# Optimization experiments

Hardware: AMD Instinct MI355X
Metric: run time of the kernel (lower is better)

Reference implementation:

```python
import jax, jax.numpy as jnp
import numpy as np

HIDDEN = 1024
NUM_HEADS = 16
HEAD_DIM = HIDDEN // NUM_HEADS
ROPE_BASE = 10000.0
LN_EPS = 1e-8


def _rope_cos_sin(seq_len, dim, dtype=jnp.float32):
    inv_freq = 1.0 / (ROPE_BASE ** (jnp.arange(0, dim, 2, dtype=jnp.float32) / dim))
    t = jnp.arange(seq_len, dtype=jnp.float32)
    freqs = jnp.einsum('i,j->ij', t, inv_freq)          # [S, dim/2]
    emb = jnp.concatenate([freqs, freqs], axis=-1)       # [S, dim]
    return jnp.cos(emb).astype(dtype), jnp.sin(emb).astype(dtype)


def _rotate_half(x):
    x1, x2 = jnp.split(x, 2, axis=-1)
    return jnp.concatenate([-x2, x1], axis=-1)


def setup_inputs() -> dict:
    key = jax.random.key(0)
    ks = jax.random.split(key, 8)
    B, S, H = 4, 2048, HIDDEN
    x = jax.random.normal(ks[0], (B, S, H), dtype=jnp.float32)
    # causal mask, True = attend
    attn_mask = jnp.tril(jnp.ones((S, S), dtype=bool))[None].repeat(B, axis=0)
    lim_p = 1.0 / np.sqrt(H)
    Wp = jax.random.uniform(ks[1], (H, 4 * H), minval=-lim_p, maxval=lim_p, dtype=jnp.float32)
    bp = jax.random.uniform(ks[2], (4 * H,), minval=-lim_p, maxval=lim_p, dtype=jnp.float32)
    ln_g = jnp.ones((H,), dtype=jnp.float32)
    ln_b = jnp.zeros((H,), dtype=jnp.float32)
    Wt = jax.random.uniform(ks[3], (H, H), minval=-lim_p, maxval=lim_p, dtype=jnp.float32)
    bt = jax.random.uniform(ks[4], (H,), minval=-lim_p, maxval=lim_p, dtype=jnp.float32)
    return {"x": x, "attn_mask": attn_mask, "Wp": Wp, "bp": bp,
            "ln_g": ln_g, "ln_b": ln_b, "Wt": Wt, "bt": bt}


def reference(x, attn_mask, Wp, bp, ln_g, ln_b, Wt, bt):
    B, S, H = x.shape
    nh, hd = NUM_HEADS, HEAD_DIM
    proj = x @ Wp + bp                                   # [B,S,4H]
    U, V, Q, K = jnp.split(proj, 4, axis=-1)
    # [B, nh, S, hd]
    Q = Q.reshape(B, S, nh, hd).transpose(0, 2, 1, 3)
    K = K.reshape(B, S, nh, hd).transpose(0, 2, 1, 3)
    V = V.reshape(B, S, nh, hd).transpose(0, 2, 1, 3)
    cos, sin = _rope_cos_sin(S, hd, x.dtype)             # [S, hd]
    Qr = Q * cos + _rotate_half(Q) * sin
    Kr = K * cos + _rotate_half(K) * sin
    scale = hd ** -0.5
    scores = jnp.einsum('bhqd,bhkd->bhqk', Qr, Kr) * scale
    # masked positions -> sigmoid(-inf) == 0; use where for grad safety
    attn = jnp.where(attn_mask[:, None, :, :], jax.nn.sigmoid(scores), 0.0)
    attn_out = jnp.einsum('bhqk,bhkd->bhqd', attn, V)
    attn_out = attn_out.transpose(0, 2, 1, 3).reshape(B, S, H)
    mu = jnp.mean(attn_out, axis=-1, keepdims=True)
    var = jnp.var(attn_out, axis=-1, keepdims=True)
    attn_out = (attn_out - mu) / jnp.sqrt(var + LN_EPS) * ln_g + ln_b
    gated = jax.nn.silu(U) * attn_out
    out = gated @ Wt + bt
    return x + out
```

## Files before the change

### kernel.cpp

```cpp
#include <hip/hip_runtime.h>
#include <math.h>

#define H 1024
#define NH 16
#define HD 64
#define B_ 4
#define S_ 2048
#define ROWS (B_*S_)

#define QSCALE (-0.1803368801111664f)
#define ROPE_C (9.210340371976184f / 32.0f)

typedef __bf16 bf16x2_t __attribute__((ext_vector_type(2)));
typedef __bf16 bf16x4_t __attribute__((ext_vector_type(4)));
typedef __bf16 bf16x8_t __attribute__((ext_vector_type(8)));
typedef float floatx4_t __attribute__((ext_vector_type(4)));

#define GLOAD_LDS16(gp, lp)                                                        \
    __builtin_amdgcn_global_load_lds(                                              \
        (const __attribute__((address_space(1))) unsigned int*)(gp),               \
        (__attribute__((address_space(3))) unsigned int*)(lp), 16, 0, 0)

__global__ __launch_bounds__(256)
void prep_kernel(const float* __restrict__ x, const float* __restrict__ Wp,
                 const float* __restrict__ Wt,
                 __bf16* __restrict__ Ax, __bf16* __restrict__ Wp_t,
                 __bf16* __restrict__ Wt_t)
{
    __shared__ __bf16 t[32][33];
    const int flat = blockIdx.x;
    const int tid = threadIdx.x;

    if (flat < 8192) {
        size_t i = (size_t)flat * 256 + tid;
        float4 v = *reinterpret_cast<const float4*>(&x[i * 4]);
        bf16x4_t w = { (__bf16)v.x, (__bf16)v.y, (__bf16)v.z, (__bf16)v.w };
        *reinterpret_cast<bf16x4_t*>(&Ax[i * 4]) = w;
        return;
    }
    const float* W; __bf16* Wo; int K, N, bn, bk;
    if (flat < 12288) {
        int id = flat - 8192;  W = Wp; Wo = Wp_t; K = 1024; N = 4096;
        bn = (id & 127) * 32;  bk = (id >> 7) * 32;
    } else {
        int id = flat - 12288; W = Wt; Wo = Wt_t; K = 1024; N = 1024;
        bn = (id & 31) * 32;   bk = (id >> 5) * 32;
    }
    const int tx = tid & 31, ty = tid >> 5;
#pragma unroll
    for (int i = 0; i < 4; i++) {
        int r = ty + i * 8;
        t[tx][r] = (__bf16)W[(size_t)(bk + r) * N + bn + tx];
    }
    __syncthreads();
#pragma unroll
    for (int i = 0; i < 4; i++) {
        int r = ty + i * 8;
        Wo[(size_t)(bn + r) * K + bk + tx] = t[r][tx];
    }
}


__global__ __launch_bounds__(256)
void gemm_out(const __bf16* __restrict__ A, const __bf16* __restrict__ Bt,
              const float* __restrict__ bias, const float* __restrict__ resid,
              float* __restrict__ C, int M, int N, int K)
{
    __shared__ __bf16 As[2][4096];
    __shared__ __bf16 Bs[2][4096];

    const int tid  = threadIdx.x;
    const int wave = tid >> 6, lane = tid & 63;
    const int quad = lane >> 4, ln = lane & 15;
    const int wm = wave & 1, wn = wave >> 1;
    const int m0 = blockIdx.y * 128, n0 = blockIdx.x * 128;

    const int srow = lane >> 2;
    const int skc  = (((lane & 3) ^ ((srow >> 1) & 3)) * 8);
    const int qsw  = (quad ^ ((ln >> 1) & 3)) * 8;

    const int i0 = wave * 2, i1 = i0 + 1;
    const size_t ga0 = (size_t)(m0 + i0 * 16 + srow) * K + skc;
    const size_t ga1 = (size_t)(m0 + i1 * 16 + srow) * K + skc;
    const size_t gb0 = (size_t)(n0 + i0 * 16 + srow) * K + skc;
    const size_t gb1 = (size_t)(n0 + i1 * 16 + srow) * K + skc;

    floatx4_t acc[4][4];
#pragma unroll
    for (int i = 0; i < 4; i++)
#pragma unroll
        for (int j = 0; j < 4; j++) acc[i][j] = (floatx4_t){0.f, 0.f, 0.f, 0.f};

    GLOAD_LDS16(A  + ga0, &As[0][i0 * 512]);
    GLOAD_LDS16(A  + ga1, &As[0][i1 * 512]);
    GLOAD_LDS16(Bt + gb0, &Bs[0][i0 * 512]);
    GLOAD_LDS16(Bt + gb1, &Bs[0][i1 * 512]);

    int buf = 0;
    for (int k0 = 0; k0 < K; k0 += 32, buf ^= 1) {
        __syncthreads();
        if (k0 + 32 < K) {
            int nb = buf ^ 1, kn = k0 + 32;
            GLOAD_LDS16(A  + ga0 + kn, &As[nb][i0 * 512]);
            GLOAD_LDS16(A  + ga1 + kn, &As[nb][i1 * 512]);
            GLOAD_LDS16(Bt + gb0 + kn, &Bs[nb][i0 * 512]);
            GLOAD_LDS16(Bt + gb1 + kn, &Bs[nb][i1 * 512]);
        }
        bf16x8_t af[4], bf[4];
#pragma unroll
        for (int mt = 0; mt < 4; mt++)
            af[mt] = *reinterpret_cast<const bf16x8_t*>(&As[buf][(wm * 64 + mt * 16 + ln) * 32 + qsw]);
#pragma unroll
        for (int nt = 0; nt < 4; nt++)
            bf[nt] = *reinterpret_cast<const bf16x8_t*>(&Bs[buf][(wn * 64 + nt * 16 + ln) * 32 + qsw]);
#pragma unroll
        for (int mt = 0; mt < 4; mt++)
#pragma unroll
            for (int nt = 0; nt < 4; nt++)
                acc[mt][nt] = __builtin_amdgcn_mfma_f32_16x16x32_bf16(af[mt], bf[nt], acc[mt][nt], 0, 0, 0);
    }

#pragma unroll
    for (int mt = 0; mt < 4; mt++) {
#pragma unroll
        for (int nt = 0; nt < 4; nt++) {
            int col = n0 + wn * 64 + nt * 16 + ln;
            float bv = bias[col];
#pragma unroll
            for (int reg = 0; reg < 4; reg++) {
                int row = m0 + wm * 64 + mt * 16 + quad * 4 + reg;
                C[(size_t)row * N + col] = acc[mt][nt][reg] + bv + resid[(size_t)row * N + col];
            }
        }
    }
}

__global__ __launch_bounds__(256)
void gemm_proj(const __bf16* __restrict__ A, const __bf16* __restrict__ Bt,
               const float* __restrict__ bias,
               __bf16* __restrict__ Ug, __bf16* __restrict__ Vh,
               __bf16* __restrict__ Qh, __bf16* __restrict__ Kh)
{
    const int K = 1024;
    __shared__ __bf16 As[2][4096];
    __shared__ __bf16 Bs[2][4096];

    const int tid  = threadIdx.x;
    const int wave = tid >> 6, lane = tid & 63;
    const int quad = lane >> 4, ln = lane & 15;
    const int wm = wave & 1, wn = wave >> 1;
    const int m0 = blockIdx.y * 128, n0 = blockIdx.x * 128;

    const int srow = lane >> 2;
    const int skc  = (((lane & 3) ^ ((srow >> 1) & 3)) * 8);
    const int qsw  = (quad ^ ((ln >> 1) & 3)) * 8;

    const int i0 = wave * 2, i1 = i0 + 1;
    const size_t ga0 = (size_t)(m0 + i0 * 16 + srow) * K + skc;
    const size_t ga1 = (size_t)(m0 + i1 * 16 + srow) * K + skc;
    const size_t gb0 = (size_t)(n0 + i0 * 16 + srow) * K + skc;
    const size_t gb1 = (size_t)(n0 + i1 * 16 + srow) * K + skc;

    floatx4_t acc[4][4];
#pragma unroll
    for (int i = 0; i < 4; i++)
#pragma unroll
        for (int j = 0; j < 4; j++) acc[i][j] = (floatx4_t){0.f, 0.f, 0.f, 0.f};

    GLOAD_LDS16(A  + ga0, &As[0][i0 * 512]);
    GLOAD_LDS16(A  + ga1, &As[0][i1 * 512]);
    GLOAD_LDS16(Bt + gb0, &Bs[0][i0 * 512]);
    GLOAD_LDS16(Bt + gb1, &Bs[0][i1 * 512]);

    int buf = 0;
    for (int k0 = 0; k0 < K; k0 += 32, buf ^= 1) {
        __syncthreads();
        if (k0 + 32 < K) {
            int nb = buf ^ 1, kn = k0 + 32;
            GLOAD_LDS16(A  + ga0 + kn, &As[nb][i0 * 512]);
            GLOAD_LDS16(A  + ga1 + kn, &As[nb][i1 * 512]);
            GLOAD_LDS16(Bt + gb0 + kn, &Bs[nb][i0 * 512]);
            GLOAD_LDS16(Bt + gb1 + kn, &Bs[nb][i1 * 512]);
        }
        bf16x8_t af[4], bf[4];
#pragma unroll
        for (int mt = 0; mt < 4; mt++)
            af[mt] = *reinterpret_cast<const bf16x8_t*>(&As[buf][(wm * 64 + mt * 16 + ln) * 32 + qsw]);
#pragma unroll
        for (int nt = 0; nt < 4; nt++)
            bf[nt] = *reinterpret_cast<const bf16x8_t*>(&Bs[buf][(wn * 64 + nt * 16 + ln) * 32 + qsw]);
#pragma unroll
        for (int mt = 0; mt < 4; mt++)
#pragma unroll
            for (int nt = 0; nt < 4; nt++)
                acc[mt][nt] = __builtin_amdgcn_mfma_f32_16x16x32_bf16(af[mt], bf[nt], acc[mt][nt], 0, 0, 0);
    }

    float bv[4];
#pragma unroll
    for (int nt = 0; nt < 4; nt++) bv[nt] = bias[n0 + wn * 64 + nt * 16 + ln];

    if (n0 < 1024) {
#pragma unroll
        for (int mt = 0; mt < 4; mt++)
#pragma unroll
            for (int nt = 0; nt < 4; nt++) {
                int col = n0 + wn * 64 + nt * 16 + ln;
#pragma unroll
                for (int reg = 0; reg < 4; reg++) {
                    int row = m0 + wm * 64 + mt * 16 + quad * 4 + reg;
                    Ug[(size_t)row * 1024 + col] = (__bf16)(acc[mt][nt][reg] + bv[nt]);
                }
            }
    } else if (n0 < 2048) {
        const int h = ((n0 - 1024) >> 6) + wn;
#pragma unroll
        for (int mt = 0; mt < 4; mt++)
#pragma unroll
            for (int reg = 0; reg < 4; reg++) {
                int row = m0 + wm * 64 + mt * 16 + quad * 4 + reg;
                int b = row >> 11, s = row & (S_ - 1);
                size_t orow = ((size_t)(b * NH + h) * S_ + s) * 64;
#pragma unroll
                for (int nt = 0; nt < 4; nt++)
                    Vh[orow + nt * 16 + ln] = (__bf16)(acc[mt][nt][reg] + bv[nt]);
            }
    } else {
        const bool isQ = (n0 < 3072);
        const int h = ((n0 - (isQ ? 2048 : 3072)) >> 6) + wn;
        __bf16* dst = isQ ? Qh : Kh;
        const float sc = isQ ? QSCALE : 1.0f;
        const float inv0 = __expf(-(float)ln * ROPE_C);
        const float inv1 = __expf(-(float)(16 + ln) * ROPE_C);
#pragma unroll
        for (int mt = 0; mt < 4; mt++)
#pragma unroll
            for (int reg = 0; reg < 4; reg++) {
                int row = m0 + wm * 64 + mt * 16 + quad * 4 + reg;
                int b = row >> 11, s = row & (S_ - 1);
                size_t orow = ((size_t)(b * NH + h) * S_ + s) * 64;
                float sn0, cs0, sn1, cs1;
                __sincosf((float)s * inv0, &sn0, &cs0);
                __sincosf((float)s * inv1, &sn1, &cs1);
                float lo0 = acc[mt][0][reg] + bv[0], hi0 = acc[mt][2][reg] + bv[2];
                float lo1 = acc[mt][1][reg] + bv[1], hi1 = acc[mt][3][reg] + bv[3];
                dst[orow + ln]      = (__bf16)((lo0 * cs0 - hi0 * sn0) * sc);
                dst[orow + 32 + ln] = (__bf16)((hi0 * cs0 + lo0 * sn0) * sc);
                dst[orow + 16 + ln] = (__bf16)((lo1 * cs1 - hi1 * sn1) * sc);
                dst[orow + 48 + ln] = (__bf16)((hi1 * cs1 + lo1 * sn1) * sc);
            }
    }
}

__global__ __launch_bounds__(256)
void transpose_v(const __bf16* __restrict__ Vh, __bf16* __restrict__ VtG)
{
    const int tid = threadIdx.x;
    const int st = blockIdx.x, bh = blockIdx.y;
    const int s0 = st * 64;
    const int d = tid & 63, k16 = tid >> 6;
    __bf16 vals[16];
#pragma unroll
    for (int j = 0; j < 16; j++) {
        int k = s0 + k16 * 16 + j;
        vals[j] = Vh[((size_t)bh * S_ + k) * 64 + d];
    }
    size_t orow = ((size_t)(bh * 64 + d)) * S_ + s0 + k16 * 16;
    *reinterpret_cast<bf16x8_t*>(&VtG[orow])     = *reinterpret_cast<bf16x8_t*>(&vals[0]);
    *reinterpret_cast<bf16x8_t*>(&VtG[orow + 8]) = *reinterpret_cast<bf16x8_t*>(&vals[8]);
}

__global__ __launch_bounds__(256)
void attn_mfma(const __bf16* __restrict__ Qh, const __bf16* __restrict__ Kh,
               const __bf16* __restrict__ VtG, __bf16* __restrict__ attn_out)
{
    __shared__ __bf16 Ks[2][4096];
    __shared__ __bf16 Vt[2][4096];
    __shared__ __bf16 Ps[4][16][72];

    const int tid = threadIdx.x, wave = tid >> 6, lane = tid & 63;
    const int quad = lane >> 4, ln = lane & 15;
    const int qt = (S_ / 128 - 1) - (blockIdx.x >> 6);
    const int hb = blockIdx.x & 63, h = hb & 15, b = hb >> 4, bh = b * NH + h;
    const int Q0 = qt * 128, T0 = 2 * qt;
    const int wl = wave * 16 + ln;

    const size_t qr = ((size_t)bh * S_ + Q0 + wl) * 64;
    bf16x8_t qa[2][2];
    qa[0][0] = *reinterpret_cast<const bf16x8_t*>(&Qh[qr + quad * 8]);
    qa[0][1] = *reinterpret_cast<const bf16x8_t*>(&Qh[qr + 32 + quad * 8]);
    qa[1][0] = *reinterpret_cast<const bf16x8_t*>(&Qh[qr + 4096 + quad * 8]);
    qa[1][1] = *reinterpret_cast<const bf16x8_t*>(&Qh[qr + 4096 + 32 + quad * 8]);

    const int sr = lane >> 3, scl = (lane & 7) ^ sr;
    const int c0 = wave * 2, c1 = c0 + 1;
    const size_t khead = (size_t)bh * S_ * 64;
    const int koff0 = (c0 * 8 + sr) * 64 + scl * 8;
    const int koff1 = (c1 * 8 + sr) * 64 + scl * 8;
    const size_t vg0 = ((size_t)bh * 64 + c0 * 8 + sr) * S_ + scl * 8;
    const size_t vg1 = ((size_t)bh * 64 + c1 * 8 + sr) * S_ + scl * 8;

    const int m7 = ln & 7;
    int ka[4][2];
#pragma unroll
    for (int nt = 0; nt < 4; nt++) {
        int row = nt * 16 + ln;
        ka[nt][0] = row * 64 + ((quad ^ m7) << 3);
        ka[nt][1] = row * 64 + (((quad + 4) ^ m7) << 3);
    }

    floatx4_t o[2][4];
#pragma unroll
    for (int s = 0; s < 2; s++)
#pragma unroll
        for (int dt = 0; dt < 4; dt++) o[s][dt] = (floatx4_t){0.f, 0.f, 0.f, 0.f};

    GLOAD_LDS16(Kh  + khead + koff0, &Ks[0][c0 * 512]);
    GLOAD_LDS16(Kh  + khead + koff1, &Ks[0][c1 * 512]);
    GLOAD_LDS16(VtG + vg0,           &Vt[0][c0 * 512]);
    GLOAD_LDS16(VtG + vg1,           &Vt[0][c1 * 512]);

    for (int kt = 0; kt <= T0 + 1; kt++) {
        const int buf = kt & 1;
        __syncthreads();
        if (kt <= T0) {
            const int nb = buf ^ 1;
            const size_t kg = khead + (size_t)(kt + 1) * 4096;
            GLOAD_LDS16(Kh  + kg + koff0,            &Ks[nb][c0 * 512]);
            GLOAD_LDS16(Kh  + kg + koff1,            &Ks[nb][c1 * 512]);
            GLOAD_LDS16(VtG + vg0 + (kt + 1) * 64,   &Vt[nb][c0 * 512]);
            GLOAD_LDS16(VtG + vg1 + (kt + 1) * 64,   &Vt[nb][c1 * 512]);
        }

        bf16x8_t kf[4][2], vf[4][2];
#pragma unroll
        for (int nt = 0; nt < 4; nt++) {
            kf[nt][0] = *reinterpret_cast<const bf16x8_t*>(&Ks[buf][ka[nt][0]]);
            kf[nt][1] = *reinterpret_cast<const bf16x8_t*>(&Ks[buf][ka[nt][1]]);
        }
#pragma unroll
        for (int dt = 0; dt < 4; dt++) {
            vf[dt][0] = *reinterpret_cast<const bf16x8_t*>(&Vt[buf][ka[dt][0]]);
            vf[dt][1] = *reinterpret_cast<const bf16x8_t*>(&Vt[buf][ka[dt][1]]);
        }

        const int mode0 = (kt < T0) ? 0 : ((kt == T0) ? 1 : 2);
        const int mode1 = (kt <= T0) ? 0 : 1;

#pragma unroll
        for (int s = 0; s < 2; s++) {
            const int mode = s ? mode1 : mode0;
            if (mode == 2) continue;

            floatx4_t st[4];
#pragma unroll
            for (int nt = 0; nt < 4; nt++) {
                floatx4_t acc = (floatx4_t){0.f, 0.f, 0.f, 0.f};
                acc = __builtin_amdgcn_mfma_f32_16x16x32_bf16(kf[nt][0], qa[s][0], acc, 0, 0, 0);
                acc = __builtin_amdgcn_mfma_f32_16x16x32_bf16(kf[nt][1], qa[s][1], acc, 0, 0, 0);
                st[nt] = acc;
            }

#pragma unroll
            for (int nt = 0; nt < 4; nt++) {
                bf16x4_t pk;
#pragma unroll
                for (int r = 0; r < 4; r++) {
                    float a = st[nt][r];
                    if (mode == 1) {
                        int kl = nt * 16 + quad * 4 + r;
                        a = (kl <= wl) ? a : __builtin_inff();
                    }
                    float p = __builtin_amdgcn_rcpf(1.f + __builtin_amdgcn_exp2f(a));
                    pk[r] = (__bf16)p;
                }
                *reinterpret_cast<bf16x4_t*>(&Ps[wave][ln][nt * 16 + quad * 4]) = pk;
            }

            const __bf16* prow = &Ps[wave][ln][quad * 8];
            bf16x8_t p0 = *reinterpret_cast<const bf16x8_t*>(prow);
            bf16x8_t p1 = *reinterpret_cast<const bf16x8_t*>(prow + 32);
#pragma unroll
            for (int dt = 0; dt < 4; dt++) {
                o[s][dt] = __builtin_amdgcn_mfma_f32_16x16x32_bf16(p0, vf[dt][0], o[s][dt], 0, 0, 0);
                o[s][dt] = __builtin_amdgcn_mfma_f32_16x16x32_bf16(p1, vf[dt][1], o[s][dt], 0, 0, 0);
            }
        }
    }

#pragma unroll
    for (int s = 0; s < 2; s++) {
        const int qrow_g = b * S_ + Q0 + s * 64 + wave * 16 + quad * 4;
#pragma unroll
        for (int dt = 0; dt < 4; dt++) {
#pragma unroll
            for (int reg = 0; reg < 4; reg++) {
                attn_out[(size_t)(qrow_g + reg) * H + h * 64 + dt * 16 + ln] =
                    (__bf16)o[s][dt][reg];
            }
        }
    }
}

__global__ __launch_bounds__(256)
void ln_gate_kernel(const __bf16* __restrict__ attn_out, const __bf16* __restrict__ Ug,
                    const float* __restrict__ ln_g, const float* __restrict__ ln_b,
                    __bf16* __restrict__ gated)
{
    const int row = blockIdx.x;
    const int tid = threadIdx.x;

    bf16x4_t vb = *reinterpret_cast<const bf16x4_t*>(&attn_out[(size_t)row * H + tid * 4]);
    float v0 = (float)vb[0], v1 = (float)vb[1], v2 = (float)vb[2], v3 = (float)vb[3];
    float s  = v0 + v1 + v2 + v3;
    float sq = v0 * v0 + v1 * v1 + v2 * v2 + v3 * v3;
#pragma unroll
    for (int off = 32; off > 0; off >>= 1) {
        s  += __shfl_down(s, off);
        sq += __shfl_down(sq, off);
    }
    __shared__ float ps[4], pq[4];
    int wave = tid >> 6, lane = tid & 63;
    if (lane == 0) { ps[wave] = s; pq[wave] = sq; }
    __syncthreads();
    float ts = ps[0] + ps[1] + ps[2] + ps[3];
    float tq = pq[0] + pq[1] + pq[2] + pq[3];
    float mu  = ts * (1.f / (float)H);
    float var = tq * (1.f / (float)H) - mu * mu;
    float rstd = rsqrtf(var + 1e-8f);

    bf16x4_t ub = *reinterpret_cast<const bf16x4_t*>(&Ug[(size_t)row * 1024 + tid * 4]);
    float4 g  = *reinterpret_cast<const float4*>(&ln_g[tid * 4]);
    float4 bb = *reinterpret_cast<const float4*>(&ln_b[tid * 4]);
    float u0 = (float)ub[0], u1 = (float)ub[1], u2 = (float)ub[2], u3 = (float)ub[3];
    bf16x4_t outv;
    outv[0] = (__bf16)(((v0 - mu) * rstd * g.x + bb.x) * (u0 / (1.f + __expf(-u0))));
    outv[1] = (__bf16)(((v1 - mu) * rstd * g.y + bb.y) * (u1 / (1.f + __expf(-u1))));
    outv[2] = (__bf16)(((v2 - mu) * rstd * g.z + bb.z) * (u2 / (1.f + __expf(-u2))));
    outv[3] = (__bf16)(((v3 - mu) * rstd * g.w + bb.w) * (u3 / (1.f + __expf(-u3))));
    *reinterpret_cast<bf16x4_t*>(&gated[(size_t)row * H + tid * 4]) = outv;
}

extern "C" void kernel_launch(void* const* d_in, const int* in_sizes, int n_in,
                              void* d_out, int out_size, void* d_ws, size_t ws_size,
                              hipStream_t stream)
{
    const float* x    = (const float*)d_in[0];
    const float* Wp   = (const float*)d_in[2];
    const float* bp   = (const float*)d_in[3];
    const float* ln_g = (const float*)d_in[4];
    const float* ln_b = (const float*)d_in[5];
    const float* Wt   = (const float*)d_in[6];
    const float* bt   = (const float*)d_in[7];
    float* out = (float*)d_out;

    char* ws = (char*)d_ws;
    const size_t MB = 1024 * 1024;
    __bf16* Ug    = (__bf16*)(ws);
    __bf16* Vh    = (__bf16*)(ws + 16  * MB);
    __bf16* Qh    = (__bf16*)(ws + 32  * MB);
    __bf16* Kh    = (__bf16*)(ws + 48  * MB);
    __bf16* attn  = (__bf16*)(ws + 64  * MB);
    __bf16* gated = (__bf16*)(ws + 80  * MB);
    __bf16* VtG   = (__bf16*)(ws + 96  * MB);
    __bf16* Ax    = (__bf16*)(ws + 112 * MB);
    __bf16* Wp_t  = (__bf16*)(ws + 128 * MB);
    __bf16* Wt_t  = (__bf16*)(ws + 136 * MB);

    prep_kernel<<<13312, 256, 0, stream>>>(x, Wp, Wt, Ax, Wp_t, Wt_t);

    dim3 g1(4096 / 128, ROWS / 128);
    gemm_proj<<<g1, 256, 0, stream>>>(Ax, Wp_t, bp, Ug, Vh, Qh, Kh);

    transpose_v<<<dim3(S_ / 64, B_ * NH), 256, 0, stream>>>(Vh, VtG);

    attn_mfma<<<(S_ / 128) * NH * B_, 256, 0, stream>>>(Qh, Kh, VtG, attn);

    ln_gate_kernel<<<ROWS, 256, 0, stream>>>(attn, Ug, ln_g, ln_b, gated);

    dim3 g3(1024 / 128, ROWS / 128);
    gemm_out<<<g3, 256, 0, stream>>>(gated, Wt_t, bt, x, out, ROWS, 1024, 1024);
}
```

Measured before the change: 343.7 us.

## Switch projection and output GEMMs to 32x32x16 MFMA with single-buffered LDS

Both GEMM kernels move from 16x16x32 to 32x32x16 bf16 MFMA instructions, so each wave holds 2x2 32x32 accumulators instead of 4x4 16x16 tiles. The aim is to cut the number of LDS fragment reads and MFMA issues per k-step. The LDS double buffer is dropped in favour of load, sync, compute, sync. That halves shared memory, which may raise occupancy, but global loads no longer overlap compute within a block. The epilogues are rewritten for the 32x32 accumulator row layout, including the RoPE pairing of columns d and d+32.

```diff
diff --git a/kernel.cpp b/kernel.cpp
--- a/kernel.cpp
+++ b/kernel.cpp
@@ -15,6 +15,7 @@
 typedef __bf16 bf16x4_t __attribute__((ext_vector_type(4)));
 typedef __bf16 bf16x8_t __attribute__((ext_vector_type(8)));
 typedef float floatx4_t __attribute__((ext_vector_type(4)));
+typedef float floatx16_t __attribute__((ext_vector_type(16)));
 
 #define GLOAD_LDS16(gp, lp)                                                        \
     __builtin_amdgcn_global_load_lds(                                              \
@@ -66,69 +67,76 @@
               const float* __restrict__ bias, const float* __restrict__ resid,
               float* __restrict__ C, int M, int N, int K)
 {
-    __shared__ __bf16 As[2][4096];
-    __shared__ __bf16 Bs[2][4096];
+    __shared__ __bf16 As[128 * 32];
+    __shared__ __bf16 Bs[128 * 32];
 
     const int tid  = threadIdx.x;
     const int wave = tid >> 6, lane = tid & 63;
-    const int quad = lane >> 4, ln = lane & 15;
+    const int l31 = lane & 31, half = lane >> 5;
     const int wm = wave & 1, wn = wave >> 1;
     const int m0 = blockIdx.y * 128, n0 = blockIdx.x * 128;
 
     const int srow = lane >> 2;
     const int skc  = (((lane & 3) ^ ((srow >> 1) & 3)) * 8);
-    const int qsw  = (quad ^ ((ln >> 1) & 3)) * 8;
-
-    const int i0 = wave * 2, i1 = i0 + 1;
-    const size_t ga0 = (size_t)(m0 + i0 * 16 + srow) * K + skc;
-    const size_t ga1 = (size_t)(m0 + i1 * 16 + srow) * K + skc;
-    const size_t gb0 = (size_t)(n0 + i0 * 16 + srow) * K + skc;
-    const size_t gb1 = (size_t)(n0 + i1 * 16 + srow) * K + skc;
-
-    floatx4_t acc[4][4];
-#pragma unroll
-    for (int i = 0; i < 4; i++)
-#pragma unroll
-        for (int j = 0; j < 4; j++) acc[i][j] = (floatx4_t){0.f, 0.f, 0.f, 0.f};
-
-    GLOAD_LDS16(A  + ga0, &As[0][i0 * 512]);
-    GLOAD_LDS16(A  + ga1, &As[0][i1 * 512]);
-    GLOAD_LDS16(Bt + gb0, &Bs[0][i0 * 512]);
-    GLOAD_LDS16(Bt + gb1, &Bs[0][i1 * 512]);
-
-    int buf = 0;
-    for (int k0 = 0; k0 < K; k0 += 32, buf ^= 1) {
+
+    const int fsw = (l31 >> 1) & 3;
+    int aoff[2][2], boff[2][2];
+#pragma unroll
+    for (int mt = 0; mt < 2; mt++)
+#pragma unroll
+        for (int ks = 0; ks < 2; ks++) {
+            int ra = wm * 64 + mt * 32 + l31;
+            int rb = wn * 64 + mt * 32 + l31;
+            int c = ks * 2 + half;
+            aoff[mt][ks] = ra * 32 + ((c ^ fsw) * 8);
+            boff[mt][ks] = rb * 32 + ((c ^ fsw) * 8);
+        }
+
+    floatx16_t acc[2][2];
+#pragma unroll
+    for (int i = 0; i < 2; i++)
+#pragma unroll
+        for (int j = 0; j < 2; j++) acc[i][j] = (floatx16_t)(0.f);
+
+    for (int k0 = 0; k0 < K; k0 += 32) {
+#pragma unroll
+        for (int p = 0; p < 2; p++) {
+            int i = wave * 2 + p;
+            int rl = i * 16 + srow;
+            GLOAD_LDS16(A  + (size_t)(m0 + rl) * K + k0 + skc, &As[i * 512]);
+            GLOAD_LDS16(Bt + (size_t)(n0 + rl) * K + k0 + skc, &Bs[i * 512]);
+        }
         __syncthreads();
-        if (k0 + 32 < K) {
-            int nb = buf ^ 1, kn = k0 + 32;
-            GLOAD_LDS16(A  + ga0 + kn, &As[nb][i0 * 512]);
-            GLOAD_LDS16(A  + ga1 + kn, &As[nb][i1 * 512]);
-            GLOAD_LDS16(Bt + gb0 + kn, &Bs[nb][i0 * 512]);
-            GLOAD_LDS16(Bt + gb1 + kn, &Bs[nb][i1 * 512]);
-        }
-        bf16x8_t af[4], bf[4];
-#pragma unroll
-        for (int mt = 0; mt < 4; mt++)
-            af[mt] = *reinterpret_cast<const bf16x8_t*>(&As[buf][(wm * 64 + mt * 16 + ln) * 32 + qsw]);
-#pragma unroll
-        for (int nt = 0; nt < 4; nt++)
-            bf[nt] = *reinterpret_cast<const bf16x8_t*>(&Bs[buf][(wn * 64 + nt * 16 + ln) * 32 + qsw]);
-#pragma unroll
-        for (int mt = 0; mt < 4; mt++)
-#pragma unroll
-            for (int nt = 0; nt < 4; nt++)
-                acc[mt][nt] = __builtin_amdgcn_mfma_f32_16x16x32_bf16(af[mt], bf[nt], acc[mt][nt], 0, 0, 0);
-    }
-
-#pragma unroll
-    for (int mt = 0; mt < 4; mt++) {
-#pragma unroll
-        for (int nt = 0; nt < 4; nt++) {
-            int col = n0 + wn * 64 + nt * 16 + ln;
+
+        bf16x8_t af[2][2], bf[2][2];
+#pragma unroll
+        for (int mt = 0; mt < 2; mt++)
+#pragma unroll
+            for (int ks = 0; ks < 2; ks++) {
+                af[mt][ks] = *reinterpret_cast<const bf16x8_t*>(&As[aoff[mt][ks]]);
+                bf[mt][ks] = *reinterpret_cast<const bf16x8_t*>(&Bs[boff[mt][ks]]);
+            }
+#pragma unroll
+        for (int ks = 0; ks < 2; ks++)
+#pragma unroll
+            for (int mt = 0; mt < 2; mt++)
+#pragma unroll
+                for (int nt = 0; nt < 2; nt++)
+                    acc[mt][nt] = __builtin_amdgcn_mfma_f32_32x32x16_bf16(
+                        af[mt][ks], bf[nt][ks], acc[mt][nt], 0, 0, 0);
+        __syncthreads();
+    }
+
+#pragma unroll
+    for (int mt = 0; mt < 2; mt++) {
+#pragma unroll
+        for (int nt = 0; nt < 2; nt++) {
+            int col = n0 + wn * 64 + nt * 32 + l31;
             float bv = bias[col];
 #pragma unroll
-            for (int reg = 0; reg < 4; reg++) {
-                int row = m0 + wm * 64 + mt * 16 + quad * 4 + reg;
+            for (int reg = 0; reg < 16; reg++) {
+                int rowf = (reg & 3) + 8 * (reg >> 2) + 4 * half;
+                int row = m0 + wm * 64 + mt * 32 + rowf;
                 C[(size_t)row * N + col] = acc[mt][nt][reg] + bv + resid[(size_t)row * N + col];
             }
         }
@@ -142,112 +150,116 @@
                __bf16* __restrict__ Qh, __bf16* __restrict__ Kh)
 {
     const int K = 1024;
-    __shared__ __bf16 As[2][4096];
-    __shared__ __bf16 Bs[2][4096];
+    __shared__ __bf16 As[128 * 32];
+    __shared__ __bf16 Bs[128 * 32];
 
     const int tid  = threadIdx.x;
     const int wave = tid >> 6, lane = tid & 63;
-    const int quad = lane >> 4, ln = lane & 15;
+    const int l31 = lane & 31, half = lane >> 5;
     const int wm = wave & 1, wn = wave >> 1;
     const int m0 = blockIdx.y * 128, n0 = blockIdx.x * 128;
 
     const int srow = lane >> 2;
     const int skc  = (((lane & 3) ^ ((srow >> 1) & 3)) * 8);
-    const int qsw  = (quad ^ ((ln >> 1) & 3)) * 8;
-
-    const int i0 = wave * 2, i1 = i0 + 1;
-    const size_t ga0 = (size_t)(m0 + i0 * 16 + srow) * K + skc;
-    const size_t ga1 = (size_t)(m0 + i1 * 16 + srow) * K + skc;
-    const size_t gb0 = (size_t)(n0 + i0 * 16 + srow) * K + skc;
-    const size_t gb1 = (size_t)(n0 + i1 * 16 + srow) * K + skc;
-
-    floatx4_t acc[4][4];
-#pragma unroll
-    for (int i = 0; i < 4; i++)
-#pragma unroll
-        for (int j = 0; j < 4; j++) acc[i][j] = (floatx4_t){0.f, 0.f, 0.f, 0.f};
-
-    GLOAD_LDS16(A  + ga0, &As[0][i0 * 512]);
-    GLOAD_LDS16(A  + ga1, &As[0][i1 * 512]);
-    GLOAD_LDS16(Bt + gb0, &Bs[0][i0 * 512]);
-    GLOAD_LDS16(Bt + gb1, &Bs[0][i1 * 512]);
-
-    int buf = 0;
-    for (int k0 = 0; k0 < K; k0 += 32, buf ^= 1) {
+
+    const int fsw = (l31 >> 1) & 3;
+    int aoff[2][2], boff[2][2];
+#pragma unroll
+    for (int mt = 0; mt < 2; mt++)
+#pragma unroll
+        for (int ks = 0; ks < 2; ks++) {
+            int ra = wm * 64 + mt * 32 + l31;
+            int rb = wn * 64 + mt * 32 + l31;
+            int c = ks * 2 + half;
+            aoff[mt][ks] = ra * 32 + ((c ^ fsw) * 8);
+            boff[mt][ks] = rb * 32 + ((c ^ fsw) * 8);
+        }
+
+    floatx16_t acc[2][2];
+#pragma unroll
+    for (int i = 0; i < 2; i++)
+#pragma unroll
+        for (int j = 0; j < 2; j++) acc[i][j] = (floatx16_t)(0.f);
+
+    for (int k0 = 0; k0 < K; k0 += 32) {
+#pragma unroll
+        for (int p = 0; p < 2; p++) {
+            int i = wave * 2 + p;
+            int rl = i * 16 + srow;
+            GLOAD_LDS16(A  + (size_t)(m0 + rl) * K + k0 + skc, &As[i * 512]);
+            GLOAD_LDS16(Bt + (size_t)(n0 + rl) * K + k0 + skc, &Bs[i * 512]);
+        }
         __syncthreads();
-        if (k0 + 32 < K) {
-            int nb = buf ^ 1, kn = k0 + 32;
-            GLOAD_LDS16(A  + ga0 + kn, &As[nb][i0 * 512]);
-            GLOAD_LDS16(A  + ga1 + kn, &As[nb][i1 * 512]);
-            GLOAD_LDS16(Bt + gb0 + kn, &Bs[nb][i0 * 512]);
-            GLOAD_LDS16(Bt + gb1 + kn, &Bs[nb][i1 * 512]);
-        }
-        bf16x8_t af[4], bf[4];
-#pragma unroll
-        for (int mt = 0; mt < 4; mt++)
-            af[mt] = *reinterpret_cast<const bf16x8_t*>(&As[buf][(wm * 64 + mt * 16 + ln) * 32 + qsw]);
-#pragma unroll
-        for (int nt = 0; nt < 4; nt++)
-            bf[nt] = *reinterpret_cast<const bf16x8_t*>(&Bs[buf][(wn * 64 + nt * 16 + ln) * 32 + qsw]);
-#pragma unroll
-        for (int mt = 0; mt < 4; mt++)
-#pragma unroll
-            for (int nt = 0; nt < 4; nt++)
-                acc[mt][nt] = __builtin_amdgcn_mfma_f32_16x16x32_bf16(af[mt], bf[nt], acc[mt][nt], 0, 0, 0);
-    }
-
-    float bv[4];
-#pragma unroll
-    for (int nt = 0; nt < 4; nt++) bv[nt] = bias[n0 + wn * 64 + nt * 16 + ln];
+
+        bf16x8_t af[2][2], bf[2][2];
+#pragma unroll
+        for (int mt = 0; mt < 2; mt++)
+#pragma unroll
+            for (int ks = 0; ks < 2; ks++) {
+                af[mt][ks] = *reinterpret_cast<const bf16x8_t*>(&As[aoff[mt][ks]]);
+                bf[mt][ks] = *reinterpret_cast<const bf16x8_t*>(&Bs[boff[mt][ks]]);
+            }
+#pragma unroll
+        for (int ks = 0; ks < 2; ks++)
+#pragma unroll
+            for (int mt = 0; mt < 2; mt++)
+#pragma unroll
+                for (int nt = 0; nt < 2; nt++)
+                    acc[mt][nt] = __builtin_amdgcn_mfma_f32_32x32x16_bf16(
+                        af[mt][ks], bf[nt][ks], acc[mt][nt], 0, 0, 0);
+        __syncthreads();
+    }
+
+    float bv[2];
+    bv[0] = bias[n0 + wn * 64 + l31];
+    bv[1] = bias[n0 + wn * 64 + 32 + l31];
 
     if (n0 < 1024) {
 #pragma unroll
-        for (int mt = 0; mt < 4; mt++)
-#pragma unroll
-            for (int nt = 0; nt < 4; nt++) {
-                int col = n0 + wn * 64 + nt * 16 + ln;
-#pragma unroll
-                for (int reg = 0; reg < 4; reg++) {
-                    int row = m0 + wm * 64 + mt * 16 + quad * 4 + reg;
+        for (int mt = 0; mt < 2; mt++)
+#pragma unroll
+            for (int nt = 0; nt < 2; nt++) {
+                int col = n0 + wn * 64 + nt * 32 + l31;
+#pragma unroll
+                for (int reg = 0; reg < 16; reg++) {
+                    int rowf = (reg & 3) + 8 * (reg >> 2) + 4 * half;
+                    int row = m0 + wm * 64 + mt * 32 + rowf;
                     Ug[(size_t)row * 1024 + col] = (__bf16)(acc[mt][nt][reg] + bv[nt]);
                 }
             }
     } else if (n0 < 2048) {
         const int h = ((n0 - 1024) >> 6) + wn;
 #pragma unroll
-        for (int mt = 0; mt < 4; mt++)
-#pragma unroll
-            for (int reg = 0; reg < 4; reg++) {
-                int row = m0 + wm * 64 + mt * 16 + quad * 4 + reg;
+        for (int mt = 0; mt < 2; mt++)
+#pragma unroll
+            for (int reg = 0; reg < 16; reg++) {
+                int rowf = (reg & 3) + 8 * (reg >> 2) + 4 * half;
+                int row = m0 + wm * 64 + mt * 32 + rowf;
                 int b = row >> 11, s = row & (S_ - 1);
                 size_t orow = ((size_t)(b * NH + h) * S_ + s) * 64;
-#pragma unroll
-                for (int nt = 0; nt < 4; nt++)
-                    Vh[orow + nt * 16 + ln] = (__bf16)(acc[mt][nt][reg] + bv[nt]);
+                Vh[orow + l31]      = (__bf16)(acc[mt][0][reg] + bv[0]);
+                Vh[orow + 32 + l31] = (__bf16)(acc[mt][1][reg] + bv[1]);
             }
     } else {
         const bool isQ = (n0 < 3072);
         const int h = ((n0 - (isQ ? 2048 : 3072)) >> 6) + wn;
         __bf16* dst = isQ ? Qh : Kh;
         const float sc = isQ ? QSCALE : 1.0f;
-        const float inv0 = __expf(-(float)ln * ROPE_C);
-        const float inv1 = __expf(-(float)(16 + ln) * ROPE_C);
-#pragma unroll
-        for (int mt = 0; mt < 4; mt++)
-#pragma unroll
-            for (int reg = 0; reg < 4; reg++) {
-                int row = m0 + wm * 64 + mt * 16 + quad * 4 + reg;
+        const float inv = __expf(-(float)l31 * ROPE_C);
+#pragma unroll
+        for (int mt = 0; mt < 2; mt++)
+#pragma unroll
+            for (int reg = 0; reg < 16; reg++) {
+                int rowf = (reg & 3) + 8 * (reg >> 2) + 4 * half;
+                int row = m0 + wm * 64 + mt * 32 + rowf;
                 int b = row >> 11, s = row & (S_ - 1);
                 size_t orow = ((size_t)(b * NH + h) * S_ + s) * 64;
-                float sn0, cs0, sn1, cs1;
-                __sincosf((float)s * inv0, &sn0, &cs0);
-                __sincosf((float)s * inv1, &sn1, &cs1);
-                float lo0 = acc[mt][0][reg] + bv[0], hi0 = acc[mt][2][reg] + bv[2];
-                float lo1 = acc[mt][1][reg] + bv[1], hi1 = acc[mt][3][reg] + bv[3];
-                dst[orow + ln]      = (__bf16)((lo0 * cs0 - hi0 * sn0) * sc);
-                dst[orow + 32 + ln] = (__bf16)((hi0 * cs0 + lo0 * sn0) * sc);
-                dst[orow + 16 + ln] = (__bf16)((lo1 * cs1 - hi1 * sn1) * sc);
-                dst[orow + 48 + ln] = (__bf16)((hi1 * cs1 + lo1 * sn1) * sc);
+                float sn, cs;
+                __sincosf((float)s * inv, &sn, &cs);
+                float lo = acc[mt][0][reg] + bv[0];
+                float hi = acc[mt][1][reg] + bv[1];
+                dst[orow + l31]      = (__bf16)((lo * cs - hi * sn) * sc);
+                dst[orow + 32 + l31] = (__bf16)((hi * cs + lo * sn) * sc);
             }
     }
 }
```

Result: no change. 337.3 us (-1.9%).
